# Kernel optimization log

Hardware: AMD Instinct MI355X
Metric: run time of the kernel (lower is better)

Reference implementation:

```python
import jax, jax.numpy as jnp
import numpy as np

D_MODEL = 1024
N_HEADS = 16
HEAD_DIM = D_MODEL // N_HEADS  # 64
SEQ = 2048
BATCH = 2


def setup_inputs() -> dict:
    key = jax.random.key(0)
    ks = jax.random.split(key, 12)
    s = 1.0 / np.sqrt(D_MODEL)
    return {
        "query": jax.random.normal(ks[0], (SEQ, BATCH, D_MODEL), jnp.float32),
        "key": jax.random.normal(ks[1], (SEQ, BATCH, D_MODEL), jnp.float32),
        "value": jax.random.normal(ks[2], (SEQ, BATCH, D_MODEL), jnp.float32),
        "Wq": jax.random.normal(ks[3], (D_MODEL, D_MODEL), jnp.float32) * s,
        "bq": jax.random.normal(ks[4], (D_MODEL,), jnp.float32) * s,
        "Wk": jax.random.normal(ks[5], (D_MODEL, D_MODEL), jnp.float32) * s,
        "bk": jax.random.normal(ks[6], (D_MODEL,), jnp.float32) * s,
        "Wv": jax.random.normal(ks[7], (D_MODEL, D_MODEL), jnp.float32) * s,
        "bv": jax.random.normal(ks[8], (D_MODEL,), jnp.float32) * s,
        "Wo": jax.random.normal(ks[9], (D_MODEL, D_MODEL), jnp.float32) * s,
        "bo": jax.random.normal(ks[10], (D_MODEL,), jnp.float32) * s,
    }


def _rope_tables(seq_len):
    # theta_i = 1 / 10000^(2i/head_dim), i in [0, head_dim//2)
    theta = 1.0 / (10000.0 ** (2.0 * jnp.arange(HEAD_DIM // 2, dtype=jnp.float32) / HEAD_DIM))
    pos = jnp.arange(seq_len, dtype=jnp.float32)[:, None, None, None] * theta  # [S,1,1,hd/2]
    return jnp.sin(pos), jnp.cos(pos)


def _apply_rope(t, sin, cos):
    # t: [S, B, H, hd]; NOTE faithful to source: t2 = q1*sin - q2*cos (minus)
    h = HEAD_DIM // 2
    q1, q2 = t[..., :h], t[..., h:]
    return jnp.concatenate([q1 * cos - q2 * sin, q1 * sin - q2 * cos], axis=-1)


def reference(query, key, value, Wq, bq, Wk, bk, Wv, bv, Wo, bo):
    S, B, _ = query.shape
    q = (query @ Wq.T + bq).reshape(S, B, N_HEADS, HEAD_DIM)
    k = (key @ Wk.T + bk).reshape(S, B, N_HEADS, HEAD_DIM)
    v = (value @ Wv.T + bv).reshape(S, B, N_HEADS, HEAD_DIM)
    sin, cos = _rope_tables(S)
    q = _apply_rope(q, sin, cos)
    k = _apply_rope(k, sin, cos)
    # [S,B,H,d] -> [B,H,S,d]
    q = q.transpose(1, 2, 0, 3)
    k = k.transpose(1, 2, 0, 3)
    v = v.transpose(1, 2, 0, 3)
    scale = 1.0 / jnp.sqrt(jnp.float32(HEAD_DIM))
    scores = jnp.einsum("bhqd,bhkd->bhqk", q, k) * scale
    attn = jax.nn.softmax(scores, axis=-1)
    out = jnp.einsum("bhqk,bhkd->bhqd", attn, v)  # [B,H,S,d]
    out = out.transpose(2, 0, 1, 3).reshape(S, B, D_MODEL)
    return out @ Wo.T + bo
```

## Files before the change

### kernel.cpp

```cpp
#include <hip/hip_runtime.h>
#include <hip/hip_bf16.h>

#define DMODEL 1024
#define NHEADS 16
#define HDIM   64
#define SEQ    2048
#define BATCH  2
#define MROWS  (SEQ*BATCH)

typedef unsigned int u32;
typedef unsigned short u16;
typedef __attribute__((ext_vector_type(8))) short bfrag;
typedef __attribute__((ext_vector_type(4))) float f32x4;
typedef __attribute__((ext_vector_type(16))) float f32x16;
typedef union { u32 u[4]; bfrag f; } fragu;

#define LOG2E 1.44269504088896341f

__device__ __forceinline__ u32 f2bf(float x) {
    unsigned u = __float_as_uint(x);
    return (u + 0x7fffu + ((u >> 16) & 1u)) >> 16;
}
__device__ __forceinline__ float bf2f(u32 h) {
    return __uint_as_float(h << 16);
}
__device__ __forceinline__ u32 pk2bf(float a, float b) {
    __hip_bfloat162 t = __float22bfloat162_rn(make_float2(a, b));
    u32 r;
    __builtin_memcpy(&r, &t, 4);
    return r;
}
__device__ __forceinline__ float fexp2(float x) {
#if __has_builtin(__builtin_amdgcn_exp2f)
    return __builtin_amdgcn_exp2f(x);
#else
    return exp2f(x);
#endif
}

__device__ __forceinline__ void gld16(const void* g, void* l) {
    __builtin_amdgcn_global_load_lds(
        (const __attribute__((address_space(1))) unsigned int*)g,
        (__attribute__((address_space(3))) unsigned int*)l, 16, 0, 0);
}


__global__ __launch_bounds__(256) void prep_kernel(
    const float* __restrict__ Wq, const float* __restrict__ Wk,
    const float* __restrict__ Wv, const float* __restrict__ Wo,
    float* __restrict__ query, float* __restrict__ key, float* __restrict__ value,
    u16* __restrict__ wqb, u16* __restrict__ wkb, u16* __restrict__ wvb,
    u16* __restrict__ wob, float2* __restrict__ tab)
{
    const int y = blockIdx.y;
    if (y == 3) {
        if (blockIdx.x >= 256) return;
        const int e = blockIdx.x * 256 + threadIdx.x;
        const int s = e >> 5, i = e & 31;
        const double th = exp(-(double)i * (9.210340371976184 / 32.0));
        double sn, cs;
        sincos((double)s * th, &sn, &cs);
        tab[e] = make_float2((float)sn, (float)cs);
        return;
    }
    const float* src;
    u16* dst;
    int nr;
    if (y < 3 || y == 7) {
        src = (y == 0) ? Wq : (y == 1) ? Wk : (y == 2) ? Wv : Wo;
        dst = (y == 0) ? wqb : (y == 1) ? wkb : (y == 2) ? wvb : wob;
        nr = 2;
    } else {
        float* io = (y == 4) ? query : (y == 5) ? key : value;
        src = io;
        dst = (u16*)io;
        nr = 8;
    }
    const int lane = threadIdx.x & 63;
    const int wv   = threadIdx.x >> 6;
    const int g8   = lane >> 3;
    const int l8   = lane & 7;
    for (int r = 0; r < nr; ++r) {
        const size_t kb = (size_t)blockIdx.x * (4 * nr) + (size_t)r * 4 + wv;
        const float4 x4 = *(const float4*)(src + kb * 256 + lane * 4);
        __align__(8) u16 hb[4];
        __align__(8) u16 lb[4];
        const float xs[4] = {x4.x, x4.y, x4.z, x4.w};
        #pragma unroll
        for (int i = 0; i < 4; ++i) {
            const u32 h = f2bf(xs[i]);
            hb[i] = (u16)h;
            lb[i] = (u16)f2bf(xs[i] - bf2f(h));
        }
        u16* o = dst + kb * 512 + g8 * 64 + l8 * 4;
        *(uint2*)o        = *(const uint2*)hb;
        *(uint2*)(o + 32) = *(const uint2*)lb;
    }
}

template <int NI>
__device__ __forceinline__ void gemm_body(
    int id, int mode,
    const u16* __restrict__ Ab, const u16* __restrict__ Wb,
    const float* __restrict__ bias, const float2* __restrict__ tab,
    float rope_scale,
    u16* __restrict__ Oh, u16* __restrict__ Ol, float* __restrict__ Of,
    u16* smem16)
{
    u16* sA = smem16;
    u16* sB = smem16 + 16384;

    const int tid   = threadIdx.x;
    const int w     = tid >> 6;
    const int lane  = tid & 63;
    const int lrow  = lane & 15;
    const int lquad = lane >> 4;

    const int NBLK = 1024 / (NI * 16);
    const int xcd  = id & 7;
    const int jj   = id >> 3;
    const int nblk = jj & (NBLK - 1);
    const int mblk = (xcd << 2) | (jj / NBLK);
    const int n0   = nblk * NI * 16;
    const int m0   = mblk * 128;

    const int srow8 = lane >> 3;
    const int sch   = (lane & 7) ^ srow8;

    int aoffh[2], aoffl[2], boffh[NI], boffl[NI];
    #pragma unroll
    for (int mi = 0; mi < 2; ++mi) {
        const int ra = w * 32 + mi * 16 + lrow;
        aoffh[mi] = ra * 64 + ((lquad ^ (ra & 7)) << 3);
        aoffl[mi] = ra * 64 + (((lquad + 4) ^ (ra & 7)) << 3);
    }
    #pragma unroll
    for (int ni = 0; ni < NI; ++ni) {
        const int rb = ni * 16 + lrow;
        boffh[ni] = rb * 64 + ((lquad ^ (rb & 7)) << 3);
        boffl[ni] = rb * 64 + (((lquad + 4) ^ (rb & 7)) << 3);
    }

    f32x4 acc[2][NI] = {};

    auto stage = [&](int t) {
        const int h = t & 1;
        #pragma unroll
        for (int i = 0; i < 4; ++i) {
            const int slab = w * 4 + i;
            const int row  = slab * 8 + srow8;
            gld16(Ab + (size_t)(m0 + row) * 2048 + t * 64 + sch * 8,
                  sA + h * 8192 + slab * 512);
        }
        #pragma unroll
        for (int i = 0; i < NI / 2; ++i) {
            const int slab = w * (NI / 2) + i;
            const int row  = slab * 8 + srow8;
            gld16(Wb + (size_t)(n0 + row) * 2048 + t * 64 + sch * 8,
                  sB + h * (NI * 1024) + slab * 512);
        }
    };

    stage(0);
    for (int t = 0; t < 32; ++t) {
        __syncthreads();
        if (t < 31) stage(t + 1);
        const int h = t & 1;
        const u16* sAh_ = sA + h * 8192;
        const u16* sBh_ = sB + h * (NI * 1024);

        bfrag ah[2], al[2], bh[NI], bl[NI];
        #pragma unroll
        for (int mi = 0; mi < 2; ++mi) {
            ah[mi] = *(const bfrag*)&sAh_[aoffh[mi]];
            al[mi] = *(const bfrag*)&sAh_[aoffl[mi]];
        }
        #pragma unroll
        for (int ni = 0; ni < NI; ++ni) {
            bh[ni] = *(const bfrag*)&sBh_[boffh[ni]];
            bl[ni] = *(const bfrag*)&sBh_[boffl[ni]];
        }

        #pragma unroll
        for (int mi = 0; mi < 2; ++mi)
            #pragma unroll
            for (int ni = 0; ni < NI; ++ni) {
                acc[mi][ni] = __builtin_amdgcn_mfma_f32_16x16x32_bf16(ah[mi], bh[ni], acc[mi][ni], 0, 0, 0);
                acc[mi][ni] = __builtin_amdgcn_mfma_f32_16x16x32_bf16(ah[mi], bl[ni], acc[mi][ni], 0, 0, 0);
                acc[mi][ni] = __builtin_amdgcn_mfma_f32_16x16x32_bf16(al[mi], bh[ni], acc[mi][ni], 0, 0, 0);
            }
    }

    float bn[NI];
    #pragma unroll
    for (int ni = 0; ni < NI; ++ni) bn[ni] = bias[n0 + ni * 16 + lrow];

    if constexpr (NI == 4) {
        if (mode == 0) {
            const int hblk = nblk;
            #pragma unroll
            for (int mi = 0; mi < 2; ++mi)
                #pragma unroll
                for (int r = 0; r < 4; ++r) {
                    const int mrow = w * 32 + mi * 16 + lquad * 4 + r;
                    const int m  = m0 + mrow;
                    const int bb = m & 1;
                    const int sg = m >> 1;
                    const size_t ob = (((size_t)(bb * NHEADS + hblk) * SEQ) + sg) * HDIM;
                    #pragma unroll
                    for (int ni = 0; ni < 2; ++ni) {
                        const int i = ni * 16 + lrow;
                        const float2 sc = tab[(size_t)sg * 32 + i];
                        const float x1 = acc[mi][ni][r]     + bn[ni];
                        const float x2 = acc[mi][ni + 2][r] + bn[ni + 2];
                        const float o1 = (x1 * sc.y - x2 * sc.x) * rope_scale;
                        const float o2 = (x1 * sc.x - x2 * sc.y) * rope_scale;
                        const u32 h1 = f2bf(o1);
                        const u32 h2 = f2bf(o2);
                        Oh[ob + i]      = (u16)h1;  Ol[ob + i]      = (u16)f2bf(o1 - bf2f(h1));
                        Oh[ob + i + 32] = (u16)h2;  Ol[ob + i + 32] = (u16)f2bf(o2 - bf2f(h2));
                    }
                }
            return;
        }
        if (mode == 1) {
            __syncthreads();
            u32* vb = (u32*)smem16;
            #pragma unroll
            for (int mi = 0; mi < 2; ++mi)
                #pragma unroll
                for (int r = 0; r < 4; ++r) {
                    const int mrow = w * 32 + mi * 16 + lquad * 4 + r;
                    const int bb = mrow & 1;
                    const int sl = mrow >> 1;
                    #pragma unroll
                    for (int ni = 0; ni < 4; ++ni) {
                        const int d = ni * 16 + lrow;
                        vb[bb * 4160 + d * 65 + sl] = f2bf(acc[mi][ni][r] + bn[ni]);
                    }
                }
            __syncthreads();
            const int hblk = nblk;
            #pragma unroll
            for (int rep = 0; rep < 4; ++rep) {
                const int c  = rep * 256 + tid;
                const int bb = c >> 9;
                const int d  = (c >> 3) & 63;
                const int s8 = c & 7;
                __align__(8) u16 hb[8];
                #pragma unroll
                for (int j = 0; j < 8; ++j)
                    hb[j] = (u16)vb[bb * 4160 + d * 65 + s8 * 8 + j];
                const size_t orow = ((size_t)(bb * NHEADS + hblk) * HDIM + d) * SEQ + (m0 >> 1);
                const int blk16 = (s8 >> 1) * 16;
                const int off   = (s8 & 1) * 4;
                *(uint2*)&Oh[orow + blk16 + off]     = *(const uint2*)&hb[0];
                *(uint2*)&Oh[orow + blk16 + 8 + off] = *(const uint2*)&hb[4];
            }
            return;
        }
    }
    #pragma unroll
    for (int mi = 0; mi < 2; ++mi)
        #pragma unroll
        for (int r = 0; r < 4; ++r) {
            const int m = m0 + w * 32 + mi * 16 + lquad * 4 + r;
            #pragma unroll
            for (int ni = 0; ni < NI; ++ni)
                Of[(size_t)m * 1024 + n0 + ni * 16 + lrow] = acc[mi][ni][r] + bn[ni];
        }
}

__global__ __launch_bounds__(256) void qkv_gemm_kernel(
    const u16* __restrict__ query, const u16* __restrict__ key,
    const u16* __restrict__ value,
    const u16* __restrict__ Wqb, const u16* __restrict__ Wkb,
    const u16* __restrict__ Wvb,
    const float* __restrict__ bq, const float* __restrict__ bk,
    const float* __restrict__ bv, const float2* __restrict__ tab,
    u16* __restrict__ Qh, u16* __restrict__ Ql,
    u16* __restrict__ Kh, u16* __restrict__ Kl,
    u16* __restrict__ VTh)
{
    __shared__ u16 smem16[24576];
    const int z  = blockIdx.z;
    const int id = blockIdx.x + 16 * blockIdx.y;
    const u16* A    = (z == 0) ? query : (z == 1) ? key : value;
    const u16* Wb   = (z == 0) ? Wqb : (z == 1) ? Wkb : Wvb;
    const float* bb = (z == 0) ? bq : (z == 1) ? bk : bv;
    u16* Oh = (z == 0) ? Qh : (z == 1) ? Kh : VTh;
    u16* Ol = (z == 0) ? Ql : (z == 1) ? Kl : nullptr;
    const int mode = (z == 2) ? 1 : 0;
    const float scale = (z == 0) ? 0.125f * LOG2E : 1.0f;
    gemm_body<4>(id, mode, A, Wb, bb, tab, scale, Oh, Ol, nullptr, smem16);
}

__global__ __launch_bounds__(256) void out_gemm_kernel(
    const u16* __restrict__ Ab, const u16* __restrict__ Wb,
    const float* __restrict__ bias, float* __restrict__ Of)
{
    __shared__ u16 smem16[24576];
    const int id = blockIdx.x + 16 * blockIdx.y;
    gemm_body<4>(id, 2, Ab, Wb, bias, nullptr, 1.0f, nullptr, nullptr, Of, smem16);
}

__global__ __launch_bounds__(256) void attn_mfma_kernel(
    const u16* __restrict__ Qh, const u16* __restrict__ Ql,
    const u16* __restrict__ Kh, const u16* __restrict__ Kl,
    const u16* __restrict__ Vh,
    float* __restrict__ O0, float* __restrict__ O1, float* __restrict__ lsum)
{
    __shared__ u16 sKh[8192], sKl[8192];
    __shared__ u16 sVh[8192];

    const int tid  = threadIdx.x;
    const int w    = tid >> 6;
    const int lane = tid & 63;
    const int l31  = lane & 31;
    const int g    = lane >> 5;
    const int z    = blockIdx.z;

    const int id = blockIdx.x + 16 * blockIdx.y;
    const int jj = id >> 3;
    const int bh = ((id & 7) << 2) | (jj >> 4);
    const int qt = jj & 15;

    const size_t qg = ((size_t)bh * SEQ + qt * 128 + w * 32 + l31) * HDIM + g * 8;
    bfrag qfh[4], qfl[4];
    #pragma unroll
    for (int ks = 0; ks < 4; ++ks) {
        qfh[ks] = *(const bfrag*)&Qh[qg + ks * 16];
        qfl[ks] = *(const bfrag*)&Ql[qg + ks * 16];
    }

    const int srow   = lane >> 3;
    const int schunk = (lane & 7) ^ srow;
    const u16* gsrc = nullptr; u16* lbase = nullptr; size_t istep = 0, ktstep = 0;
    if (w == 0) {
        gsrc = Kh + ((size_t)bh * SEQ + srow) * HDIM + schunk * 8;
        istep = 8 * 64; ktstep = 64 * 64; lbase = sKh;
    } else if (w == 1) {
        gsrc = Kl + ((size_t)bh * SEQ + srow) * HDIM + schunk * 8;
        istep = 8 * 64; ktstep = 64 * 64; lbase = sKl;
    } else if (w == 2) {
        gsrc = Vh + ((size_t)bh * HDIM + srow) * SEQ + schunk * 8;
        istep = 8 * SEQ; ktstep = 64; lbase = sVh;
    }

    int koff[2][4];
    #pragma unroll
    for (int a = 0; a < 2; ++a) {
        const int row = a * 32 + l31;
        #pragma unroll
        for (int c = 0; c < 4; ++c)
            koff[a][c] = row * 64 + (((c * 2 + g) ^ (row & 7)) << 3);
    }

    f32x16 accO[2] = {};
    float l_loc = 0.0f;

    auto stage = [&](int kt) {
        if (w < 3) {
            const u16* gp = gsrc + (size_t)kt * ktstep;
            u16* dst = lbase + (kt & 1) * 4096;
            #pragma unroll
            for (int i = 0; i < 8; ++i)
                gld16(gp + (size_t)i * istep, dst + i * 512);
        }
    };

    const int kt0 = z * 16;
    stage(kt0);
    for (int kt = kt0; kt < kt0 + 16; ++kt) {
        __syncthreads();
        if (kt < kt0 + 15) stage(kt + 1);
        const int po = (kt & 1) * 4096;

        f32x16 accS[2] = {};
        #pragma unroll
        for (int kg = 0; kg < 2; ++kg)
            #pragma unroll
            for (int ks = 0; ks < 4; ++ks) {
                const bfrag kh_ = *(const bfrag*)&sKh[po + koff[kg][ks]];
                const bfrag kl_ = *(const bfrag*)&sKl[po + koff[kg][ks]];
                accS[kg] = __builtin_amdgcn_mfma_f32_32x32x16_bf16(kh_, qfh[ks], accS[kg], 0, 0, 0);
                accS[kg] = __builtin_amdgcn_mfma_f32_32x32x16_bf16(kh_, qfl[ks], accS[kg], 0, 0, 0);
                accS[kg] = __builtin_amdgcn_mfma_f32_32x32x16_bf16(kl_, qfh[ks], accS[kg], 0, 0, 0);
            }

        float pv[2][16];
        #pragma unroll
        for (int kg = 0; kg < 2; ++kg)
            #pragma unroll
            for (int r = 0; r < 16; ++r) {
                const float p = fexp2(accS[kg][r]);
                pv[kg][r] = p;
                l_loc += p;
            }

        #pragma unroll
        for (int kp = 0; kp < 4; ++kp) {
            const int kg = kp >> 1;
            const int t8 = (kp & 1) * 8;
            fragu ph;
            #pragma unroll
            for (int j2 = 0; j2 < 4; ++j2)
                ph.u[j2] = pk2bf(pv[kg][t8 + 2 * j2], pv[kg][t8 + 2 * j2 + 1]);
            #pragma unroll
            for (int dt = 0; dt < 2; ++dt) {
                const bfrag vh = *(const bfrag*)&sVh[po + koff[dt][kp]];
                accO[dt] = __builtin_amdgcn_mfma_f32_32x32x16_bf16(vh, ph.f, accO[dt], 0, 0, 0);
            }
        }
    }

    const float ls = l_loc + __shfl_xor(l_loc, 32);

    const int b = bh >> 4;
    const int h = bh & 15;
    const int sg = qt * 128 + w * 32 + l31;
    const int rm = sg * BATCH + b;
    if (lane < 32)
        lsum[(size_t)z * 65536 + (size_t)bh * 2048 + sg] = ls;
    float* Op = z ? O1 : O0;
    #pragma unroll
    for (int dt = 0; dt < 2; ++dt)
        #pragma unroll
        for (int rq = 0; rq < 4; ++rq) {
            float4 v4;
            v4.x = accO[dt][rq * 4 + 0];
            v4.y = accO[dt][rq * 4 + 1];
            v4.z = accO[dt][rq * 4 + 2];
            v4.w = accO[dt][rq * 4 + 3];
            *(float4*)&Op[(size_t)rm * 1024 + (h * 2 + dt) * 32 + 8 * rq + 4 * g] = v4;
        }
}

__global__ __launch_bounds__(256) void combine_kernel(
    float* __restrict__ O0, const float* __restrict__ O1,
    const float* __restrict__ lsum)
{
    const int lane = threadIdx.x & 63;
    const int wv   = threadIdx.x >> 6;
    const int g8   = lane >> 3;
    const int l8   = lane & 7;
    #pragma unroll
    for (int r = 0; r < 8; ++r) {
        const size_t kb = (size_t)blockIdx.x * 32 + (size_t)r * 4 + wv;
        const int rm = (int)(kb >> 2);
        const int t  = ((int)kb & 3) * 8 + g8;
        const int b  = rm & 1;
        const int sg = rm >> 1;
        const int h  = t >> 1;
        const float l0 = lsum[(size_t)(b * 16 + h) * 2048 + sg];
        const float l1 = lsum[65536 + (size_t)(b * 16 + h) * 2048 + sg];
        const float inv = 1.0f / (l0 + l1);
        const float4 x0 = *(const float4*)(O0 + kb * 256 + lane * 4);
        const float4 x1 = *(const float4*)(O1 + kb * 256 + lane * 4);
        const float xs[4] = {x0.x + x1.x, x0.y + x1.y, x0.z + x1.z, x0.w + x1.w};
        __align__(8) u16 hb[4];
        __align__(8) u16 lb[4];
        #pragma unroll
        for (int i = 0; i < 4; ++i) {
            const float v = xs[i] * inv;
            const u32 hh = f2bf(v);
            hb[i] = (u16)hh;
            lb[i] = (u16)f2bf(v - bf2f(hh));
        }
        u16* o = (u16*)O0 + kb * 512 + g8 * 64 + l8 * 4;
        *(uint2*)o        = *(const uint2*)hb;
        *(uint2*)(o + 32) = *(const uint2*)lb;
    }
}

extern "C" void kernel_launch(void* const* d_in, const int* in_sizes, int n_in,
                              void* d_out, int out_size, void* d_ws, size_t ws_size,
                              hipStream_t stream)
{
    float* query = (float*)d_in[0];
    float* key   = (float*)d_in[1];
    float* value = (float*)d_in[2];
    const float* Wq    = (const float*)d_in[3];
    const float* bq    = (const float*)d_in[4];
    const float* Wk    = (const float*)d_in[5];
    const float* bk    = (const float*)d_in[6];
    const float* Wv    = (const float*)d_in[7];
    const float* bv    = (const float*)d_in[8];
    const float* Wo    = (const float*)d_in[9];
    const float* bo    = (const float*)d_in[10];
    float* out = (float*)d_out;

    char* wsb = (char*)d_ws;
    const size_t MB = 1024 * 1024;
    u16* Wqb = (u16*)(wsb + 0 * MB);
    u16* Wkb = (u16*)(wsb + 4 * MB);
    u16* Wvb = (u16*)(wsb + 8 * MB);
    float2* tab = (float2*)(wsb + 12 * MB);
    u16* Qh  = (u16*)(wsb + 16 * MB); u16* Ql  = (u16*)(wsb + 24 * MB);
    u16* Kh  = (u16*)(wsb + 32 * MB); u16* Kl  = (u16*)(wsb + 40 * MB);
    u16* VTh = (u16*)(wsb + 48 * MB);
    u16* Wob = (u16*)(wsb + 56 * MB);
    float* O0   = (float*)(wsb + 0 * MB);
    float* O1   = out;
    float* lsum = (float*)(wsb + 60 * MB);

    prep_kernel<<<dim3(512, 8), 256, 0, stream>>>(
        Wq, Wk, Wv, Wo, query, key, value, Wqb, Wkb, Wvb, Wob, tab);
    qkv_gemm_kernel<<<dim3(16, 32, 3), 256, 0, stream>>>(
        (const u16*)query, (const u16*)key, (const u16*)value,
        Wqb, Wkb, Wvb, bq, bk, bv, tab, Qh, Ql, Kh, Kl, VTh);
    attn_mfma_kernel<<<dim3(16, 32, 2), 256, 0, stream>>>(
        Qh, Ql, Kh, Kl, VTh, O0, O1, lsum);
    combine_kernel<<<dim3(512), 256, 0, stream>>>(O0, O1, lsum);
    out_gemm_kernel<<<dim3(16, 32), 256, 0, stream>>>((const u16*)O0, Wob, bo, out);
}
```

Baseline: 332.0 us.

## Replace QKV GEMM with 256x128-tile, 512-thread, triple-buffered kernel

Adds a dedicated QKV projection kernel using 256x128 output tiles per 8-wave block, a three-stage cp.async-style LDS ring with explicit vmcnt waits, and setprio around MFMA bursts. Larger tiles raise operand reuse and cut global traffic versus the prior 128x64 tiles, and the deeper pipeline hides load latency. The epilogues for RoPE and the V transpose are adapted to cover two heads per block, with the V transpose done in two passes through LDS. Cost: 144KB LDS per block limits occupancy to one block per CU and grid shrinks to 384 blocks.

```diff
diff --git a/kernel.cpp b/kernel.cpp
--- a/kernel.cpp
+++ b/kernel.cpp
@@ -98,6 +98,209 @@
     }
 }
 
+__global__ __launch_bounds__(512) void qkv8_gemm_kernel(
+    const u16* __restrict__ query, const u16* __restrict__ key,
+    const u16* __restrict__ value,
+    const u16* __restrict__ Wqb, const u16* __restrict__ Wkb,
+    const u16* __restrict__ Wvb,
+    const float* __restrict__ bq, const float* __restrict__ bk,
+    const float* __restrict__ bv, const float2* __restrict__ tab,
+    u16* __restrict__ Qh, u16* __restrict__ Ql,
+    u16* __restrict__ Kh, u16* __restrict__ Kl,
+    u16* __restrict__ VTh)
+{
+    __shared__ u16 smem[73728];
+
+    const int z  = blockIdx.z;
+    const u16* Ab   = (z == 0) ? query : (z == 1) ? key : value;
+    const u16* Wb   = (z == 0) ? Wqb : (z == 1) ? Wkb : Wvb;
+    const float* bias = (z == 0) ? bq : (z == 1) ? bk : bv;
+    u16* Oh = (z == 0) ? Qh : (z == 1) ? Kh : VTh;
+    u16* Ol = (z == 0) ? Ql : (z == 1) ? Kl : nullptr;
+    const float rope_scale = (z == 0) ? 0.125f * LOG2E : 1.0f;
+    const int mode = (z == 2) ? 1 : 0;
+
+    const int tid   = threadIdx.x;
+    const int w     = tid >> 6;
+    const int wr    = w >> 1;
+    const int wc    = w & 1;
+    const int lane  = tid & 63;
+    const int lrow  = lane & 15;
+    const int lquad = lane >> 4;
+
+    const int id   = blockIdx.x + 16 * blockIdx.y;
+    const int xcd  = id & 7;
+    const int jj   = id >> 3;
+    const int nblk = jj & 7;
+    const int mblk = (xcd << 1) | (jj >> 3);
+    const int n0   = nblk * 128;
+    const int m0   = mblk * 256;
+
+    const int srow8 = lane >> 3;
+    const int sch   = (lane & 7) ^ srow8;
+
+    int aoffh[4], aoffl[4], boffh[4], boffl[4];
+    #pragma unroll
+    for (int mi = 0; mi < 4; ++mi) {
+        const int ra = wr * 64 + mi * 16 + lrow;
+        aoffh[mi] = ra * 64 + ((lquad ^ (ra & 7)) << 3);
+        aoffl[mi] = ra * 64 + (((lquad + 4) ^ (ra & 7)) << 3);
+    }
+    #pragma unroll
+    for (int ni = 0; ni < 4; ++ni) {
+        const int rb = wc * 64 + ni * 16 + lrow;
+        boffh[ni] = rb * 64 + ((lquad ^ (rb & 7)) << 3);
+        boffl[ni] = rb * 64 + (((lquad + 4) ^ (rb & 7)) << 3);
+    }
+
+    f32x4 acc[4][4] = {};
+
+    auto stage = [&](int t) {
+        u16* bufA = smem + (t % 3) * 24576;
+        u16* bufB = bufA + 16384;
+        #pragma unroll
+        for (int i = 0; i < 4; ++i) {
+            const int slab = w * 4 + i;
+            const int row  = slab * 8 + srow8;
+            gld16(Ab + (size_t)(m0 + row) * 2048 + t * 64 + sch * 8,
+                  bufA + slab * 512);
+        }
+        #pragma unroll
+        for (int i = 0; i < 2; ++i) {
+            const int slab = w * 2 + i;
+            const int row  = slab * 8 + srow8;
+            gld16(Wb + (size_t)(n0 + row) * 2048 + t * 64 + sch * 8,
+                  bufB + slab * 512);
+        }
+    };
+
+    stage(0);
+    stage(1);
+    for (int t = 0; t < 32; ++t) {
+        const u16* bA = smem + (t % 3) * 24576;
+        const u16* bB = bA + 16384;
+
+        if (t < 30) {
+            stage(t + 2);
+            asm volatile("s_waitcnt vmcnt(12)" ::: "memory");
+        } else if (t == 30) {
+            asm volatile("s_waitcnt vmcnt(6)" ::: "memory");
+        } else {
+            asm volatile("s_waitcnt vmcnt(0)" ::: "memory");
+        }
+        __builtin_amdgcn_s_barrier();
+
+        bfrag bh[4], bl[4], ah[2], al[2];
+        #pragma unroll
+        for (int ni = 0; ni < 4; ++ni) {
+            bh[ni] = *(const bfrag*)&bB[boffh[ni]];
+            bl[ni] = *(const bfrag*)&bB[boffl[ni]];
+        }
+        #pragma unroll
+        for (int mi = 0; mi < 2; ++mi) {
+            ah[mi] = *(const bfrag*)&bA[aoffh[mi]];
+            al[mi] = *(const bfrag*)&bA[aoffl[mi]];
+        }
+        __builtin_amdgcn_s_setprio(1);
+        #pragma unroll
+        for (int mi = 0; mi < 2; ++mi)
+            #pragma unroll
+            for (int ni = 0; ni < 4; ++ni) {
+                acc[mi][ni] = __builtin_amdgcn_mfma_f32_16x16x32_bf16(ah[mi], bh[ni], acc[mi][ni], 0, 0, 0);
+                acc[mi][ni] = __builtin_amdgcn_mfma_f32_16x16x32_bf16(ah[mi], bl[ni], acc[mi][ni], 0, 0, 0);
+                acc[mi][ni] = __builtin_amdgcn_mfma_f32_16x16x32_bf16(al[mi], bh[ni], acc[mi][ni], 0, 0, 0);
+            }
+        __builtin_amdgcn_s_setprio(0);
+        __builtin_amdgcn_s_barrier();
+
+        #pragma unroll
+        for (int mi = 0; mi < 2; ++mi) {
+            ah[mi] = *(const bfrag*)&bA[aoffh[2 + mi]];
+            al[mi] = *(const bfrag*)&bA[aoffl[2 + mi]];
+        }
+        __builtin_amdgcn_s_setprio(1);
+        #pragma unroll
+        for (int mi = 0; mi < 2; ++mi)
+            #pragma unroll
+            for (int ni = 0; ni < 4; ++ni) {
+                acc[2 + mi][ni] = __builtin_amdgcn_mfma_f32_16x16x32_bf16(ah[mi], bh[ni], acc[2 + mi][ni], 0, 0, 0);
+                acc[2 + mi][ni] = __builtin_amdgcn_mfma_f32_16x16x32_bf16(ah[mi], bl[ni], acc[2 + mi][ni], 0, 0, 0);
+                acc[2 + mi][ni] = __builtin_amdgcn_mfma_f32_16x16x32_bf16(al[mi], bh[ni], acc[2 + mi][ni], 0, 0, 0);
+            }
+        __builtin_amdgcn_s_setprio(0);
+        __builtin_amdgcn_s_barrier();
+    }
+
+    float bn[4];
+    #pragma unroll
+    for (int ni = 0; ni < 4; ++ni) bn[ni] = bias[n0 + wc * 64 + ni * 16 + lrow];
+
+    if (mode == 0) {
+        const int head = nblk * 2 + wc;
+        #pragma unroll
+        for (int mi = 0; mi < 4; ++mi)
+            #pragma unroll
+            for (int r = 0; r < 4; ++r) {
+                const int mrow = wr * 64 + mi * 16 + lquad * 4 + r;
+                const int m  = m0 + mrow;
+                const int bb = m & 1;
+                const int sg = m >> 1;
+                const size_t ob = (((size_t)(bb * NHEADS + head) * SEQ) + sg) * HDIM;
+                #pragma unroll
+                for (int ni = 0; ni < 2; ++ni) {
+                    const int i = ni * 16 + lrow;
+                    const float2 sc = tab[(size_t)sg * 32 + i];
+                    const float x1 = acc[mi][ni][r]     + bn[ni];
+                    const float x2 = acc[mi][ni + 2][r] + bn[ni + 2];
+                    const float o1 = (x1 * sc.y - x2 * sc.x) * rope_scale;
+                    const float o2 = (x1 * sc.x - x2 * sc.y) * rope_scale;
+                    const u32 h1 = f2bf(o1);
+                    const u32 h2 = f2bf(o2);
+                    Oh[ob + i]      = (u16)h1;  Ol[ob + i]      = (u16)f2bf(o1 - bf2f(h1));
+                    Oh[ob + i + 32] = (u16)h2;  Ol[ob + i + 32] = (u16)f2bf(o2 - bf2f(h2));
+                }
+            }
+        return;
+    }
+    __syncthreads();
+    u32* vb = (u32*)smem;
+    for (int p = 0; p < 2; ++p) {
+        if (p) __syncthreads();
+        #pragma unroll
+        for (int mi = 0; mi < 4; ++mi)
+            #pragma unroll
+            for (int r = 0; r < 4; ++r) {
+                const int mrow = wr * 64 + mi * 16 + lquad * 4 + r;
+                if ((mrow & 1) == p) {
+                    const int sl = mrow >> 1;
+                    #pragma unroll
+                    for (int ni = 0; ni < 4; ++ni) {
+                        const int d = wc * 64 + ni * 16 + lrow;
+                        vb[d * 129 + sl] = f2bf(acc[mi][ni][r] + bn[ni]);
+                    }
+                }
+            }
+        __syncthreads();
+        #pragma unroll
+        for (int rep = 0; rep < 4; ++rep) {
+            const int c  = rep * 512 + tid;
+            const int d  = c >> 4;
+            const int s8 = c & 15;
+            __align__(8) u16 hb[8];
+            #pragma unroll
+            for (int j = 0; j < 8; ++j)
+                hb[j] = (u16)vb[d * 129 + s8 * 8 + j];
+            const int head = nblk * 2 + (d >> 6);
+            const int dd   = d & 63;
+            const size_t orow = ((size_t)(p * NHEADS + head) * HDIM + dd) * SEQ + (m0 >> 1);
+            const int blk16 = (s8 >> 1) * 16;
+            const int off   = (s8 & 1) * 4;
+            *(uint2*)&Oh[orow + blk16 + off]     = *(const uint2*)&hb[0];
+            *(uint2*)&Oh[orow + blk16 + 8 + off] = *(const uint2*)&hb[4];
+        }
+    }
+}
+
 template <int NI>
 __device__ __forceinline__ void gemm_body(
     int id, int mode,
@@ -195,71 +398,6 @@
     #pragma unroll
     for (int ni = 0; ni < NI; ++ni) bn[ni] = bias[n0 + ni * 16 + lrow];
 
-    if constexpr (NI == 4) {
-        if (mode == 0) {
-            const int hblk = nblk;
-            #pragma unroll
-            for (int mi = 0; mi < 2; ++mi)
-                #pragma unroll
-                for (int r = 0; r < 4; ++r) {
-                    const int mrow = w * 32 + mi * 16 + lquad * 4 + r;
-                    const int m  = m0 + mrow;
-                    const int bb = m & 1;
-                    const int sg = m >> 1;
-                    const size_t ob = (((size_t)(bb * NHEADS + hblk) * SEQ) + sg) * HDIM;
-                    #pragma unroll
-                    for (int ni = 0; ni < 2; ++ni) {
-                        const int i = ni * 16 + lrow;
-                        const float2 sc = tab[(size_t)sg * 32 + i];
-                        const float x1 = acc[mi][ni][r]     + bn[ni];
-                        const float x2 = acc[mi][ni + 2][r] + bn[ni + 2];
-                        const float o1 = (x1 * sc.y - x2 * sc.x) * rope_scale;
-                        const float o2 = (x1 * sc.x - x2 * sc.y) * rope_scale;
-                        const u32 h1 = f2bf(o1);
-                        const u32 h2 = f2bf(o2);
-                        Oh[ob + i]      = (u16)h1;  Ol[ob + i]      = (u16)f2bf(o1 - bf2f(h1));
-                        Oh[ob + i + 32] = (u16)h2;  Ol[ob + i + 32] = (u16)f2bf(o2 - bf2f(h2));
-                    }
-                }
-            return;
-        }
-        if (mode == 1) {
-            __syncthreads();
-            u32* vb = (u32*)smem16;
-            #pragma unroll
-            for (int mi = 0; mi < 2; ++mi)
-                #pragma unroll
-                for (int r = 0; r < 4; ++r) {
-                    const int mrow = w * 32 + mi * 16 + lquad * 4 + r;
-                    const int bb = mrow & 1;
-                    const int sl = mrow >> 1;
-                    #pragma unroll
-                    for (int ni = 0; ni < 4; ++ni) {
-                        const int d = ni * 16 + lrow;
-                        vb[bb * 4160 + d * 65 + sl] = f2bf(acc[mi][ni][r] + bn[ni]);
-                    }
-                }
-            __syncthreads();
-            const int hblk = nblk;
-            #pragma unroll
-            for (int rep = 0; rep < 4; ++rep) {
-                const int c  = rep * 256 + tid;
-                const int bb = c >> 9;
-                const int d  = (c >> 3) & 63;
-                const int s8 = c & 7;
-                __align__(8) u16 hb[8];
-                #pragma unroll
-                for (int j = 0; j < 8; ++j)
-                    hb[j] = (u16)vb[bb * 4160 + d * 65 + s8 * 8 + j];
-                const size_t orow = ((size_t)(bb * NHEADS + hblk) * HDIM + d) * SEQ + (m0 >> 1);
-                const int blk16 = (s8 >> 1) * 16;
-                const int off   = (s8 & 1) * 4;
-                *(uint2*)&Oh[orow + blk16 + off]     = *(const uint2*)&hb[0];
-                *(uint2*)&Oh[orow + blk16 + 8 + off] = *(const uint2*)&hb[4];
-            }
-            return;
-        }
-    }
     #pragma unroll
     for (int mi = 0; mi < 2; ++mi)
         #pragma unroll
@@ -269,30 +407,6 @@
             for (int ni = 0; ni < NI; ++ni)
                 Of[(size_t)m * 1024 + n0 + ni * 16 + lrow] = acc[mi][ni][r] + bn[ni];
         }
-}
-
-__global__ __launch_bounds__(256) void qkv_gemm_kernel(
-    const u16* __restrict__ query, const u16* __restrict__ key,
-    const u16* __restrict__ value,
-    const u16* __restrict__ Wqb, const u16* __restrict__ Wkb,
-    const u16* __restrict__ Wvb,
-    const float* __restrict__ bq, const float* __restrict__ bk,
-    const float* __restrict__ bv, const float2* __restrict__ tab,
-    u16* __restrict__ Qh, u16* __restrict__ Ql,
-    u16* __restrict__ Kh, u16* __restrict__ Kl,
-    u16* __restrict__ VTh)
-{
-    __shared__ u16 smem16[24576];
-    const int z  = blockIdx.z;
-    const int id = blockIdx.x + 16 * blockIdx.y;
-    const u16* A    = (z == 0) ? query : (z == 1) ? key : value;
-    const u16* Wb   = (z == 0) ? Wqb : (z == 1) ? Wkb : Wvb;
-    const float* bb = (z == 0) ? bq : (z == 1) ? bk : bv;
-    u16* Oh = (z == 0) ? Qh : (z == 1) ? Kh : VTh;
-    u16* Ol = (z == 0) ? Ql : (z == 1) ? Kl : nullptr;
-    const int mode = (z == 2) ? 1 : 0;
-    const float scale = (z == 0) ? 0.125f * LOG2E : 1.0f;
-    gemm_body<4>(id, mode, A, Wb, bb, tab, scale, Oh, Ol, nullptr, smem16);
 }
 
 __global__ __launch_bounds__(256) void out_gemm_kernel(
@@ -506,7 +620,7 @@
 
     prep_kernel<<<dim3(512, 8), 256, 0, stream>>>(
         Wq, Wk, Wv, Wo, query, key, value, Wqb, Wkb, Wvb, Wob, tab);
-    qkv_gemm_kernel<<<dim3(16, 32, 3), 256, 0, stream>>>(
+    qkv8_gemm_kernel<<<dim3(16, 8, 3), 512, 0, stream>>>(
         (const u16*)query, (const u16*)key, (const u16*)value,
         Wqb, Wkb, Wvb, bq, bk, bv, tab, Qh, Ql, Kh, Kl, VTh);
     attn_mfma_kernel<<<dim3(16, 32, 2), 256, 0, stream>>>(
```

Measured after the change: 331.4 us. About the same (-0.2%).
